# Optimization experiments

Measured on AMD Instinct MI355X. Metric: run time of the kernel, lower is better.

The kernel has to match this reference:

```python
import jax, jax.numpy as jnp
import numpy as np

N, L, I, H, D = 8192, 8, 256, 512, 8
PER = N // D  # nodes per depth level; level 0 nodes are tree roots


def setup_inputs() -> dict:
    key = jax.random.key(0)
    ks = jax.random.split(key, 9)
    s = 0.05
    x_seq = jax.random.normal(ks[0], (N, L, I), jnp.float32)
    # GRU params (torch nn.GRU layout, gate order r,z,n), stored transposed [in, 3H]
    W_ih = jax.random.normal(ks[1], (I, 3 * H), jnp.float32) * s
    W_hh = jax.random.normal(ks[2], (H, 3 * H), jnp.float32) * s
    b_ih = jax.random.normal(ks[3], (3 * H,), jnp.float32) * s
    b_hh = jax.random.normal(ks[4], (3 * H,), jnp.float32) * s
    # Child-sum TreeLSTM params: x-projections for i,o,u,f and recurrent U's
    Wx = jax.random.normal(ks[5], (H, 4 * H), jnp.float32) * s
    bx = jax.random.normal(ks[6], (4 * H,), jnp.float32) * s
    U_iou = jax.random.normal(ks[7], (H, 3 * H), jnp.float32) * s
    U_f = jax.random.normal(ks[8], (H, H), jnp.float32) * s
    # Forest structure: D levels of PER nodes; node at level d>0 has a random
    # parent at level d-1; roots (level 0) point at themselves (contribution is
    # zero because their own state is still zero when level 0 is processed).
    rng = np.random.default_rng(0)
    depth = np.repeat(np.arange(D), PER).astype(np.int32)
    parent = np.arange(N, dtype=np.int32)
    for d in range(1, D):
        parent[d * PER:(d + 1) * PER] = rng.integers((d - 1) * PER, d * PER, PER)
    root_ids = np.arange(PER, dtype=np.int32)
    return {
        "x_seq": x_seq, "W_ih": W_ih, "W_hh": W_hh, "b_ih": b_ih, "b_hh": b_hh,
        "Wx": Wx, "bx": bx, "U_iou": U_iou, "U_f": U_f,
        "parent": jnp.asarray(parent), "depth": jnp.asarray(depth),
        "root_ids": jnp.asarray(root_ids), "n_levels": D,
    }


def reference(x_seq, W_ih, W_hh, b_ih, b_hh, Wx, bx, U_iou, U_f,
              parent, depth, root_ids, n_levels):
    n = x_seq.shape[0]
    h_dim = W_hh.shape[0]

    # --- GRU over each node's encoding sequence (all nodes batched) ---
    def gru_step(h, x_t):  # h: [N,H], x_t: [N,I]
        gi = x_t @ W_ih + b_ih
        gh = h @ W_hh + b_hh
        ir, iz, inn = jnp.split(gi, 3, axis=-1)
        hr, hz, hn = jnp.split(gh, 3, axis=-1)
        r = jax.nn.sigmoid(ir + hr)
        z = jax.nn.sigmoid(iz + hz)
        ng = jnp.tanh(inn + r * hn)
        return (1.0 - z) * ng + z * h, None

    h0 = jnp.zeros((n, h_dim), x_seq.dtype)
    enc, _ = jax.lax.scan(gru_step, h0, jnp.swapaxes(x_seq, 0, 1))  # [N,H]

    # --- Child-sum TreeLSTM, processed leaves -> roots by depth level ---
    xg = enc @ Wx + bx  # [N,4H]
    xi, xo, xu, xf = jnp.split(xg, 4, axis=-1)
    c = jnp.zeros((n, h_dim), x_seq.dtype)
    h = jnp.zeros((n, h_dim), x_seq.dtype)
    for level in range(n_levels - 1, -1, -1):
        h_sum = jax.ops.segment_sum(h, parent, num_segments=n)  # sum over children
        giou = h_sum @ U_iou
        i = jax.nn.sigmoid(xi + giou[:, :h_dim])
        o = jax.nn.sigmoid(xo + giou[:, h_dim:2 * h_dim])
        u = jnp.tanh(xu + giou[:, 2 * h_dim:])
        # per-child forget gate uses parent's x projection and child's h
        f = jax.nn.sigmoid(xf[parent] + h @ U_f)
        fc = jax.ops.segment_sum(f * c, parent, num_segments=n)
        c_new = i * u + fc
        mask = (depth == level)[:, None]
        c = jnp.where(mask, c_new, c)
        h = jnp.where(mask, o * jnp.tanh(c_new), h)

    # root states per tree, stacked as [2, n_trees, H] -> (c_root, h_root)
    return jnp.stack([c[root_ids], h[root_ids]])
```

## Files before the change

### kernel.cpp

```cpp
#include <hip/hip_runtime.h>
#include <math.h>

typedef short bf16x8 __attribute__((ext_vector_type(8)));
typedef float f32x4 __attribute__((ext_vector_type(4)));

__device__ __forceinline__ float sigf(float x) {
    return __builtin_amdgcn_rcpf(1.f + __expf(-x));
}
__device__ __forceinline__ float tanhf_fast(float x) {
    const float e = __expf(2.f * x);
    return 1.f - 2.f * __builtin_amdgcn_rcpf(e + 1.f);
}

__device__ __forceinline__ unsigned short f2bf(float f) {
    union { float f; unsigned u; } v; v.f = f;
    unsigned r = (v.u + 0x7FFFu + ((v.u >> 16) & 1u)) >> 16;
    return (unsigned short)r;
}
__device__ __forceinline__ float bf2f(unsigned short u) {
    union { unsigned u; float f; } v; v.u = ((unsigned)u) << 16; return v.f;
}

__device__ __forceinline__ void gload16(const unsigned short* g, unsigned short* l) {
    __builtin_amdgcn_global_load_lds(
        (const __attribute__((address_space(1))) void*)g,
        (__attribute__((address_space(3))) void*)l, 16, 0, 0);
}

__device__ __forceinline__ int swz(int slot, int row) {
    return (slot ^ ((row >> 1) & 3)) * 8;
}

__global__ void cvt_f32_bf16(const float* __restrict__ src,
                             unsigned short* __restrict__ dst, int n)
{
    const int i = (blockIdx.x * blockDim.x + threadIdx.x) * 4;
    if (i >= n) return;
    const float4 v = *reinterpret_cast<const float4*>(src + i);
    ushort4 o;
    o.x = f2bf(v.x); o.y = f2bf(v.y); o.z = f2bf(v.z); o.w = f2bf(v.w);
    *reinterpret_cast<ushort4*>(dst + i) = o;
}

__global__ void transpose_cvt(const float* __restrict__ src,
                              unsigned short* __restrict__ dst,
                              int rows, int cols)
{
    __shared__ float tile[32][33];
    const int bc = blockIdx.x * 32, br = blockIdx.y * 32;
    const int tx = threadIdx.x, ty = threadIdx.y;
    #pragma unroll
    for (int i = 0; i < 32; i += 8)
        tile[ty + i][tx] = src[(size_t)(br + ty + i) * cols + bc + tx];
    __syncthreads();
    #pragma unroll
    for (int i = 0; i < 32; i += 8)
        dst[(size_t)(bc + ty + i) * rows + br + tx] = f2bf(tile[tx][ty + i]);
}

__global__ __launch_bounds__(256, 4)
void gru_mfma(const unsigned short* __restrict__ xb, int t,
              const unsigned short* __restrict__ hbi,
              unsigned short* __restrict__ hbo,
              const unsigned short* __restrict__ WihT,
              const unsigned short* __restrict__ WhhT,
              const float* __restrict__ b_ih, const float* __restrict__ b_hh)
{
    constexpr int I = 256, H = 512, LI = 2048;
    const int m0 = blockIdx.x * 64, j0 = blockIdx.y * 64;
    const int tid = (int)threadIdx.x, lane = tid & 63, wid = tid >> 6;
    const int wm = wid >> 1, wn = wid & 1;
    const int fr = lane & 15, kg = lane >> 4;
    const int lrow = lane >> 2;
    const int scol = swz(lane & 3, lrow);

    __shared__ unsigned short smem[2 * 8192];

    f32x4 ar[2][2], az[2][2], an[2][2], ah[2][2];
    #pragma unroll
    for (int i = 0; i < 2; ++i)
        #pragma unroll
        for (int j = 0; j < 2; ++j) {
            ar[i][j] = (f32x4){0.f, 0.f, 0.f, 0.f};
            az[i][j] = (f32x4){0.f, 0.f, 0.f, 0.f};
            an[i][j] = (f32x4){0.f, 0.f, 0.f, 0.f};
            ah[i][j] = (f32x4){0.f, 0.f, 0.f, 0.f};
        }

    constexpr int nkt1 = I / 32;
    constexpr int nkt = (I + H) / 32;

    auto stage = [&](int buf, int kt) {
        const bool s1 = (kt < nkt1);
        const int k0 = s1 ? kt * 32 : (kt - nkt1) * 32;
        unsigned short* base = &smem[buf * 8192];
        #pragma unroll
        for (int q = 0; q < 4; ++q) {
            const int c = wid * 4 + q;
            if (c < 4) {
                const int row = c * 16 + lrow;
                const unsigned short* g = s1
                    ? xb + (size_t)(m0 + row) * LI + t * I + k0 + scol
                    : hbi + (size_t)(m0 + row) * H + k0 + scol;
                gload16(g, base + c * 512);
            } else {
                const int bc = c - 4, gi = bc >> 2;
                const int row = (bc & 3) * 16 + lrow;
                const unsigned short* g = s1
                    ? WihT + (size_t)(gi * H + j0 + row) * I + k0 + scol
                    : WhhT + (size_t)(gi * H + j0 + row) * H + k0 + scol;
                gload16(g, base + c * 512);
            }
        }
    };

    stage(0, 0); stage(1, 1);

    for (int kt = 0; kt < nkt; ++kt) {
        if (kt + 1 < nkt) asm volatile("s_waitcnt vmcnt(4)" ::: "memory");
        else              asm volatile("s_waitcnt vmcnt(0)" ::: "memory");
        __builtin_amdgcn_s_barrier();

        const unsigned short* sb = &smem[(kt & 1) * 8192];
        bf16x8 af[2], bfr[2], bfz[2], bfn[2];
        #pragma unroll
        for (int mi = 0; mi < 2; ++mi) {
            const int row = wm * 32 + mi * 16 + fr;
            af[mi] = *reinterpret_cast<const bf16x8*>(&sb[row * 32 + swz(kg, row)]);
        }
        #pragma unroll
        for (int ni = 0; ni < 2; ++ni) {
            const int row = wn * 32 + ni * 16 + fr;
            const int sw = swz(kg, row);
            bfr[ni] = *reinterpret_cast<const bf16x8*>(&sb[2048 + (row) * 32 + sw]);
            bfz[ni] = *reinterpret_cast<const bf16x8*>(&sb[2048 + (64 + row) * 32 + sw]);
            bfn[ni] = *reinterpret_cast<const bf16x8*>(&sb[2048 + (128 + row) * 32 + sw]);
        }
        asm volatile("s_waitcnt lgkmcnt(0)" ::: "memory");
        __builtin_amdgcn_s_barrier();
        if (kt + 2 < nkt) stage(kt & 1, kt + 2);

        const bool p1 = (kt < nkt1);
        __builtin_amdgcn_s_setprio(1);
        #pragma unroll
        for (int mi = 0; mi < 2; ++mi)
            #pragma unroll
            for (int ni = 0; ni < 2; ++ni) {
                ar[mi][ni] = __builtin_amdgcn_mfma_f32_16x16x32_bf16(af[mi], bfr[ni], ar[mi][ni], 0, 0, 0);
                az[mi][ni] = __builtin_amdgcn_mfma_f32_16x16x32_bf16(af[mi], bfz[ni], az[mi][ni], 0, 0, 0);
                if (p1)
                    an[mi][ni] = __builtin_amdgcn_mfma_f32_16x16x32_bf16(af[mi], bfn[ni], an[mi][ni], 0, 0, 0);
                else
                    ah[mi][ni] = __builtin_amdgcn_mfma_f32_16x16x32_bf16(af[mi], bfn[ni], ah[mi][ni], 0, 0, 0);
            }
        __builtin_amdgcn_s_setprio(0);
    }

    #pragma unroll
    for (int ni = 0; ni < 2; ++ni) {
        const int j = j0 + wn * 32 + ni * 16 + fr;
        const float bir = b_ih[j],         bhr = b_hh[j];
        const float biz = b_ih[H + j],     bhz = b_hh[H + j];
        const float bin = b_ih[2 * H + j], bhn = b_hh[2 * H + j];
        #pragma unroll
        for (int mi = 0; mi < 2; ++mi) {
            #pragma unroll
            for (int r = 0; r < 4; ++r) {
                const int m = m0 + wm * 32 + mi * 16 + kg * 4 + r;
                const float rg = sigf(ar[mi][ni][r] + bir + bhr);
                const float zg = sigf(az[mi][ni][r] + biz + bhz);
                const float ng = tanhf_fast(an[mi][ni][r] + bin + rg * (ah[mi][ni][r] + bhn));
                const size_t off = (size_t)m * H + j;
                const float hv = bf2f(hbi[off]);
                hbo[off] = f2bf((1.f - zg) * ng + zg * hv);
            }
        }
    }
}

__global__ __launch_bounds__(256)
void mfma_gemm128(const unsigned short* __restrict__ A,
                  const unsigned short* __restrict__ BT,
                  const float* __restrict__ bias,
                  float* __restrict__ C, int M, int N, int K)
{
    const int m0 = blockIdx.x * 128, n0 = blockIdx.y * 128;
    const int tid = (int)threadIdx.x, lane = tid & 63, wid = tid >> 6;
    const int wm = wid >> 1, wn = wid & 1;
    const int fr = lane & 15, kg = lane >> 4;
    const int lrow = lane >> 2;
    const int scol = swz(lane & 3, lrow);

    __shared__ unsigned short smem[3 * 8192];

    f32x4 acc[4][4];
    #pragma unroll
    for (int i = 0; i < 4; ++i)
        #pragma unroll
        for (int j = 0; j < 4; ++j)
            acc[i][j] = (f32x4){0.f, 0.f, 0.f, 0.f};

    auto stage = [&](int buf, int kt) {
        const int k0 = kt * 32;
        unsigned short* base = &smem[buf * 8192];
        #pragma unroll
        for (int q = 0; q < 4; ++q) {
            const int c = wid * 4 + q;
            const unsigned short* g = (c < 8)
                ? A + (size_t)(m0 + c * 16 + lrow) * K + k0 + scol
                : BT + (size_t)(n0 + (c - 8) * 16 + lrow) * K + k0 + scol;
            gload16(g, base + c * 512);
        }
    };

    const int nkt = K >> 5;
    stage(0, 0); stage(1, 1); stage(2, 2);
    int cur = 0;

    for (int kt = 0; kt < nkt; ++kt) {
        if (kt + 2 < nkt)      asm volatile("s_waitcnt vmcnt(8)" ::: "memory");
        else if (kt + 1 < nkt) asm volatile("s_waitcnt vmcnt(4)" ::: "memory");
        else                   asm volatile("s_waitcnt vmcnt(0)" ::: "memory");
        __builtin_amdgcn_s_barrier();

        const unsigned short* sb = &smem[cur * 8192];
        bf16x8 af[4], bf[4];
        #pragma unroll
        for (int mi = 0; mi < 4; ++mi) {
            const int row = wm * 64 + mi * 16 + fr;
            af[mi] = *reinterpret_cast<const bf16x8*>(&sb[row * 32 + swz(kg, row)]);
        }
        #pragma unroll
        for (int ni = 0; ni < 4; ++ni) {
            const int row = wn * 64 + ni * 16 + fr;
            bf[ni] = *reinterpret_cast<const bf16x8*>(&sb[4096 + row * 32 + swz(kg, row)]);
        }
        asm volatile("s_waitcnt lgkmcnt(0)" ::: "memory");
        __builtin_amdgcn_s_barrier();
        if (kt + 3 < nkt) stage(cur, kt + 3);

        __builtin_amdgcn_s_setprio(1);
        #pragma unroll
        for (int mi = 0; mi < 4; ++mi)
            #pragma unroll
            for (int ni = 0; ni < 4; ++ni)
                acc[mi][ni] = __builtin_amdgcn_mfma_f32_16x16x32_bf16(
                    af[mi], bf[ni], acc[mi][ni], 0, 0, 0);
        __builtin_amdgcn_s_setprio(0);
        cur = (cur == 2) ? 0 : cur + 1;
    }

    #pragma unroll
    for (int ni = 0; ni < 4; ++ni) {
        const int n = n0 + wn * 64 + ni * 16 + fr;
        const float bv = bias ? bias[n] : 0.f;
        #pragma unroll
        for (int mi = 0; mi < 4; ++mi)
            #pragma unroll
            for (int r = 0; r < 4; ++r) {
                const int m = m0 + wm * 64 + mi * 16 + kg * 4 + r;
                C[(size_t)m * N + n] = acc[mi][ni][r] + bv;
            }
    }
}

__global__ __launch_bounds__(256, 4)
void tree_gemm(const unsigned short* __restrict__ hTb,
               const unsigned short* __restrict__ UcombT,
               const float* __restrict__ xg,
               const float* __restrict__ cT,
               const int* __restrict__ parent,
               int cstart, int pstart,
               float* __restrict__ giou,
               float* __restrict__ fcs)
{
    constexpr int H = 512, N4H = 2048, G3H = 1536;
    const int m0 = blockIdx.x * 64, n0 = blockIdx.y * 64;
    const int tid = (int)threadIdx.x, lane = tid & 63, wid = tid >> 6;
    const int wm = wid >> 1, wn = wid & 1;
    const int fr = lane & 15, kg = lane >> 4;
    const int lrow = lane >> 2;
    const int scol = swz(lane & 3, lrow);

    __shared__ unsigned short smem[3 * 4096];

    f32x4 acc[2][2];
    #pragma unroll
    for (int i = 0; i < 2; ++i)
        #pragma unroll
        for (int j = 0; j < 2; ++j)
            acc[i][j] = (f32x4){0.f, 0.f, 0.f, 0.f};

    auto stage = [&](int buf, int kt) {
        const int k0 = kt * 32;
        unsigned short* base = &smem[buf * 4096];
        #pragma unroll
        for (int q = 0; q < 2; ++q) {
            const int c = wid * 2 + q;
            const unsigned short* g = (c < 4)
                ? hTb + (size_t)(cstart + m0 + c * 16 + lrow) * H + k0 + scol
                : UcombT + (size_t)(n0 + (c - 4) * 16 + lrow) * H + k0 + scol;
            gload16(g, base + c * 512);
        }
    };

    constexpr int nkt = H / 32;
    stage(0, 0); stage(1, 1); stage(2, 2);
    int cur = 0;

    for (int kt = 0; kt < nkt; ++kt) {
        if (kt + 2 < nkt)      asm volatile("s_waitcnt vmcnt(4)" ::: "memory");
        else if (kt + 1 < nkt) asm volatile("s_waitcnt vmcnt(2)" ::: "memory");
        else                   asm volatile("s_waitcnt vmcnt(0)" ::: "memory");
        __builtin_amdgcn_s_barrier();

        const unsigned short* sb = &smem[cur * 4096];
        bf16x8 af[2], bf[2];
        #pragma unroll
        for (int mi = 0; mi < 2; ++mi) {
            const int row = wm * 32 + mi * 16 + fr;
            af[mi] = *reinterpret_cast<const bf16x8*>(&sb[row * 32 + swz(kg, row)]);
        }
        #pragma unroll
        for (int ni = 0; ni < 2; ++ni) {
            const int row = wn * 32 + ni * 16 + fr;
            bf[ni] = *reinterpret_cast<const bf16x8*>(&sb[2048 + row * 32 + swz(kg, row)]);
        }
        asm volatile("s_waitcnt lgkmcnt(0)" ::: "memory");
        __builtin_amdgcn_s_barrier();
        if (kt + 3 < nkt) stage(cur, kt + 3);

        __builtin_amdgcn_s_setprio(1);
        #pragma unroll
        for (int mi = 0; mi < 2; ++mi)
            #pragma unroll
            for (int ni = 0; ni < 2; ++ni)
                acc[mi][ni] = __builtin_amdgcn_mfma_f32_16x16x32_bf16(
                    af[mi], bf[ni], acc[mi][ni], 0, 0, 0);
        __builtin_amdgcn_s_setprio(0);
        cur = (cur == 2) ? 0 : cur + 1;
    }

    if (n0 < G3H) {
        #pragma unroll
        for (int mi = 0; mi < 2; ++mi)
            #pragma unroll
            for (int r = 0; r < 4; ++r) {
                const int m = m0 + wm * 32 + mi * 16 + kg * 4 + r;
                const int p = parent[cstart + m] - pstart;
                #pragma unroll
                for (int ni = 0; ni < 2; ++ni) {
                    const int n = n0 + wn * 32 + ni * 16 + fr;
                    atomicAdd(&giou[(size_t)p * G3H + n], acc[mi][ni][r]);
                }
            }
    } else {
        #pragma unroll
        for (int mi = 0; mi < 2; ++mi)
            #pragma unroll
            for (int r = 0; r < 4; ++r) {
                const int m = m0 + wm * 32 + mi * 16 + kg * 4 + r;
                const int child = cstart + m;
                const int p = parent[child];
                #pragma unroll
                for (int ni = 0; ni < 2; ++ni) {
                    const int jf = n0 + wn * 32 + ni * 16 + fr - G3H;
                    const float f = sigf(acc[mi][ni][r] + xg[(size_t)p * N4H + G3H + jf]);
                    atomicAdd(&fcs[(size_t)(p - pstart) * H + jf],
                              f * cT[(size_t)child * H + jf]);
                }
            }
    }
}

__global__ void level_update(const float* __restrict__ xg,
                             float* __restrict__ giou,
                             float* __restrict__ fcs,
                             float* __restrict__ cT, float* __restrict__ hT,
                             unsigned short* __restrict__ hb, int pstart)
{
    constexpr int H = 512, N4H = 2048, G3H = 1536;
    const int idx = blockIdx.x * blockDim.x + threadIdx.x;
    const int pi = idx >> 9, j = idx & (H - 1);
    const int p = pstart + pi;
    const size_t xb4 = (size_t)p * N4H;
    const size_t gb = (size_t)pi * G3H;
    const float ig = sigf(xg[xb4 + j] + giou[gb + j]);
    const float og = sigf(xg[xb4 + H + j] + giou[gb + H + j]);
    const float ug = tanhf_fast(xg[xb4 + 2 * H + j] + giou[gb + 2 * H + j]);
    const float cn = ig * ug + fcs[idx];
    const float hn = og * tanhf_fast(cn);
    const size_t off = (size_t)p * H + j;
    cT[off] = cn;
    hT[off] = hn;
    hb[off] = f2bf(hn);
    giou[gb + j] = 0.f;
    giou[gb + H + j] = 0.f;
    giou[gb + 2 * H + j] = 0.f;
    fcs[idx] = 0.f;
}

__global__ void gather_out_kernel(const float* __restrict__ c,
                                  const float* __restrict__ h,
                                  const int* __restrict__ root_ids,
                                  int nroot, float* __restrict__ out)
{
    constexpr int H = 512;
    const int idx = blockIdx.x * blockDim.x + threadIdx.x;
    const int t = idx >> 9, j = idx & (H - 1);
    const int rid = root_ids[t];
    out[idx] = c[(size_t)rid * H + j];
    out[(size_t)nroot * H + idx] = h[(size_t)rid * H + j];
}

extern "C" void kernel_launch(void* const* d_in, const int* in_sizes, int n_in,
                              void* d_out, int out_size, void* d_ws, size_t ws_size,
                              hipStream_t stream)
{
    const float* x_seq = (const float*)d_in[0];
    const float* W_ih  = (const float*)d_in[1];
    const float* W_hh  = (const float*)d_in[2];
    const float* b_ih  = (const float*)d_in[3];
    const float* b_hh  = (const float*)d_in[4];
    const float* Wx    = (const float*)d_in[5];
    const float* bx    = (const float*)d_in[6];
    const float* U_iou = (const float*)d_in[7];
    const float* U_f   = (const float*)d_in[8];
    const int* parent  = (const int*)d_in[9];
    const int* root_ids = (const int*)d_in[11];

    const int threeH = in_sizes[3];
    const int H   = threeH / 3;
    const int I   = in_sizes[1] / threeH;
    const int N   = in_sizes[9];
    const int L   = in_sizes[0] / (N * I);
    const int PER = in_sizes[11];
    const int D   = N / PER;

    const size_t NH = (size_t)N * H;
    const size_t PH = (size_t)PER * H;

    char* p = (char*)d_ws;
    const size_t zone_sz = ((size_t)N * 4 * H * 4 > (size_t)N * L * I * 2)
                         ? (size_t)N * 4 * H * 4 : (size_t)N * L * I * 2;
    unsigned short* xb = (unsigned short*)p;
    float* xg = (float*)p;                       p += zone_sz;
    unsigned short* hb0 = (unsigned short*)p;    p += NH * 2;
    unsigned short* hb1 = (unsigned short*)p;    p += NH * 2;
    float* cT = (float*)p;                       p += NH * 4;
    float* hT = (float*)p;                       p += NH * 4;
    unsigned short* WihT = (unsigned short*)p;   p += (size_t)threeH * I * 2;
    unsigned short* WhhT = (unsigned short*)p;   p += (size_t)threeH * H * 2;
    unsigned short* WxT  = (unsigned short*)p;   p += (size_t)4 * H * H * 2;
    unsigned short* UcombT = (unsigned short*)p; p += (size_t)4 * H * H * 2;
    float* giou = (float*)p;                     p += PH * 3 * 4;
    float* fcs  = (float*)p;                     p += PH * 4;
    if ((size_t)(p - (char*)d_ws) > ws_size) return;

    {
        const int n = N * L * I;
        cvt_f32_bf16<<<(n / 4 + 255) / 256, 256, 0, stream>>>(x_seq, xb, n);
        dim3 blk(32, 8);
        transpose_cvt<<<dim3(threeH / 32, I / 32), blk, 0, stream>>>(W_ih, WihT, I, threeH);
        transpose_cvt<<<dim3(threeH / 32, H / 32), blk, 0, stream>>>(W_hh, WhhT, H, threeH);
        transpose_cvt<<<dim3(4 * H / 32, H / 32), blk, 0, stream>>>(Wx, WxT, H, 4 * H);
        transpose_cvt<<<dim3(threeH / 32, H / 32), blk, 0, stream>>>(U_iou, UcombT, H, threeH);
        transpose_cvt<<<dim3(H / 32, H / 32), blk, 0, stream>>>(
            U_f, UcombT + (size_t)threeH * H, H, H);
    }
    hipMemsetAsync(hb0, 0, NH * 2, stream);
    hipMemsetAsync(giou, 0, PH * 4 * 4, stream);

    {
        dim3 grid(N / 64, H / 64);
        for (int t = 0; t < L; ++t) {
            const unsigned short* hin = (t & 1) ? hb1 : hb0;
            unsigned short* hout = (t & 1) ? hb0 : hb1;
            gru_mfma<<<grid, 256, 0, stream>>>(xb, t, hin, hout,
                                               WihT, WhhT, b_ih, b_hh);
        }
    }

    mfma_gemm128<<<dim3(N / 128, 4 * H / 128), 256, 0, stream>>>(
        hb0, WxT, bx, xg, N, 4 * H, H);

    unsigned short* hTb = hb1;
    const int pw_blocks = (int)(PH / 256);

    for (int lvl = D - 1; lvl >= 0; --lvl) {
        const int pstart = lvl * PER;
        const int cstart = (lvl + 1) * PER;

        if (lvl < D - 1)
            tree_gemm<<<dim3(PER / 64, (4 * H) / 64), 256, 0, stream>>>(
                hTb, UcombT, xg, cT, parent, cstart, pstart, giou, fcs);

        level_update<<<pw_blocks, 256, 0, stream>>>(xg, giou, fcs, cT, hT,
                                                    hTb, pstart);
    }

    gather_out_kernel<<<pw_blocks, 256, 0, stream>>>(cT, hT, root_ids, PER,
                                                     (float*)d_out);
}
```

Before: 504.0 us.

## Hoist GRU input projection into one batched GEMM and store projections in bf16

```diff
diff --git a/kernel.cpp b/kernel.cpp
--- a/kernel.cpp
+++ b/kernel.cpp
@@ -29,6 +29,9 @@
 
 __device__ __forceinline__ int swz(int slot, int row) {
     return (slot ^ ((row >> 1) & 3)) * 8;
+}
+__device__ __forceinline__ int tix(int ml, int jl) {
+    return ((ml >> 4) * 2 + (jl >> 5)) * 512 + (ml & 15) * 32 + (jl & 31);
 }
 
 __global__ void cvt_f32_bf16(const float* __restrict__ src,
@@ -58,57 +61,145 @@
         dst[(size_t)(bc + ty + i) * rows + br + tx] = f2bf(tile[tx][ty + i]);
 }
 
+__global__ __launch_bounds__(256)
+void gemm_bf16out(const unsigned short* __restrict__ A,
+                  const unsigned short* __restrict__ BT,
+                  const float* __restrict__ bias,
+                  unsigned short* __restrict__ Cb, int M, int N, int K)
+{
+    const int m0 = blockIdx.x * 128, n0 = blockIdx.y * 128;
+    const int tid = (int)threadIdx.x, lane = tid & 63, wid = tid >> 6;
+    const int wm = wid >> 1, wn = wid & 1;
+    const int fr = lane & 15, kg = lane >> 4;
+    const int lrow = lane >> 2;
+    const int scol = swz(lane & 3, lrow);
+
+    __shared__ unsigned short smem[3 * 8192];
+
+    f32x4 acc[4][4];
+    #pragma unroll
+    for (int i = 0; i < 4; ++i)
+        #pragma unroll
+        for (int j = 0; j < 4; ++j)
+            acc[i][j] = (f32x4){0.f, 0.f, 0.f, 0.f};
+
+    auto stage = [&](int buf, int kt) {
+        const int k0 = kt * 32;
+        unsigned short* base = &smem[buf * 8192];
+        #pragma unroll
+        for (int q = 0; q < 4; ++q) {
+            const int c = wid * 4 + q;
+            const unsigned short* g = (c < 8)
+                ? A + (size_t)(m0 + c * 16 + lrow) * K + k0 + scol
+                : BT + (size_t)(n0 + (c - 8) * 16 + lrow) * K + k0 + scol;
+            gload16(g, base + c * 512);
+        }
+    };
+
+    const int nkt = K >> 5;
+    stage(0, 0); stage(1, 1); stage(2, 2);
+    int cur = 0;
+
+    for (int kt = 0; kt < nkt; ++kt) {
+        if (kt + 2 < nkt)      asm volatile("s_waitcnt vmcnt(8)" ::: "memory");
+        else if (kt + 1 < nkt) asm volatile("s_waitcnt vmcnt(4)" ::: "memory");
+        else                   asm volatile("s_waitcnt vmcnt(0)" ::: "memory");
+        __builtin_amdgcn_s_barrier();
+
+        const unsigned short* sb = &smem[cur * 8192];
+        bf16x8 af[4], bf[4];
+        #pragma unroll
+        for (int mi = 0; mi < 4; ++mi) {
+            const int row = wm * 64 + mi * 16 + fr;
+            af[mi] = *reinterpret_cast<const bf16x8*>(&sb[row * 32 + swz(kg, row)]);
+        }
+        #pragma unroll
+        for (int ni = 0; ni < 4; ++ni) {
+            const int row = wn * 64 + ni * 16 + fr;
+            bf[ni] = *reinterpret_cast<const bf16x8*>(&sb[4096 + row * 32 + swz(kg, row)]);
+        }
+        asm volatile("s_waitcnt lgkmcnt(0)" ::: "memory");
+        __builtin_amdgcn_s_barrier();
+        if (kt + 3 < nkt) stage(cur, kt + 3);
+
+        __builtin_amdgcn_s_setprio(1);
+        #pragma unroll
+        for (int mi = 0; mi < 4; ++mi)
+            #pragma unroll
+            for (int ni = 0; ni < 4; ++ni)
+                acc[mi][ni] = __builtin_amdgcn_mfma_f32_16x16x32_bf16(
+                    af[mi], bf[ni], acc[mi][ni], 0, 0, 0);
+        __builtin_amdgcn_s_setprio(0);
+        cur = (cur == 2) ? 0 : cur + 1;
+    }
+
+    #pragma unroll
+    for (int ni = 0; ni < 4; ++ni) {
+        const int nl = wn * 64 + ni * 16 + fr;
+        const float bv = bias[n0 + nl];
+        #pragma unroll
+        for (int mi = 0; mi < 4; ++mi)
+            #pragma unroll
+            for (int r = 0; r < 4; ++r) {
+                const int ml = wm * 64 + mi * 16 + kg * 4 + r;
+                smem[ml * 128 + nl] = f2bf(acc[mi][ni][r] + bv);
+            }
+    }
+    __syncthreads();
+    #pragma unroll
+    for (int e = 0; e < 8; ++e) {
+        const int id = tid + e * 256;
+        const int row = id >> 4, cw = id & 15;
+        const int4 v = *reinterpret_cast<const int4*>(&smem[row * 128 + cw * 8]);
+        *reinterpret_cast<int4*>(&Cb[(size_t)(m0 + row) * N + n0 + cw * 8]) = v;
+    }
+}
+
 __global__ __launch_bounds__(256, 4)
-void gru_mfma(const unsigned short* __restrict__ xb, int t,
+void gru_step(const unsigned short* __restrict__ gi,
+              int t,
               const unsigned short* __restrict__ hbi,
               unsigned short* __restrict__ hbo,
-              const unsigned short* __restrict__ WihT,
               const unsigned short* __restrict__ WhhT,
-              const float* __restrict__ b_ih, const float* __restrict__ b_hh)
-{
-    constexpr int I = 256, H = 512, LI = 2048;
+              const float* __restrict__ b_hh)
+{
+    constexpr int H = 512, G3H = 1536, L = 8;
     const int m0 = blockIdx.x * 64, j0 = blockIdx.y * 64;
     const int tid = (int)threadIdx.x, lane = tid & 63, wid = tid >> 6;
     const int wm = wid >> 1, wn = wid & 1;
     const int fr = lane & 15, kg = lane >> 4;
     const int lrow = lane >> 2;
     const int scol = swz(lane & 3, lrow);
+    const int ucol = (lane & 3) * 8;
 
     __shared__ unsigned short smem[2 * 8192];
 
-    f32x4 ar[2][2], az[2][2], an[2][2], ah[2][2];
+    f32x4 ar[2][2], az[2][2], ah[2][2];
     #pragma unroll
     for (int i = 0; i < 2; ++i)
         #pragma unroll
         for (int j = 0; j < 2; ++j) {
             ar[i][j] = (f32x4){0.f, 0.f, 0.f, 0.f};
             az[i][j] = (f32x4){0.f, 0.f, 0.f, 0.f};
-            an[i][j] = (f32x4){0.f, 0.f, 0.f, 0.f};
             ah[i][j] = (f32x4){0.f, 0.f, 0.f, 0.f};
         }
 
-    constexpr int nkt1 = I / 32;
-    constexpr int nkt = (I + H) / 32;
+    constexpr int nkt = H / 32;
 
     auto stage = [&](int buf, int kt) {
-        const bool s1 = (kt < nkt1);
-        const int k0 = s1 ? kt * 32 : (kt - nkt1) * 32;
+        const int k0 = kt * 32;
         unsigned short* base = &smem[buf * 8192];
         #pragma unroll
         for (int q = 0; q < 4; ++q) {
             const int c = wid * 4 + q;
             if (c < 4) {
-                const int row = c * 16 + lrow;
-                const unsigned short* g = s1
-                    ? xb + (size_t)(m0 + row) * LI + t * I + k0 + scol
-                    : hbi + (size_t)(m0 + row) * H + k0 + scol;
+                const unsigned short* g =
+                    hbi + (size_t)(m0 + c * 16 + lrow) * H + k0 + scol;
                 gload16(g, base + c * 512);
             } else {
-                const int bc = c - 4, gi = bc >> 2;
-                const int row = (bc & 3) * 16 + lrow;
-                const unsigned short* g = s1
-                    ? WihT + (size_t)(gi * H + j0 + row) * I + k0 + scol
-                    : WhhT + (size_t)(gi * H + j0 + row) * H + k0 + scol;
+                const int gate = (c - 4) >> 2, rowg = (c - 4) & 3;
+                const unsigned short* g =
+                    WhhT + (size_t)(gate * H + j0 + rowg * 16 + lrow) * H + k0 + scol;
                 gload16(g, base + c * 512);
             }
         }
@@ -140,7 +231,6 @@
         __builtin_amdgcn_s_barrier();
         if (kt + 2 < nkt) stage(kt & 1, kt + 2);
 
-        const bool p1 = (kt < nkt1);
         __builtin_amdgcn_s_setprio(1);
         #pragma unroll
         for (int mi = 0; mi < 2; ++mi)
@@ -148,126 +238,83 @@
             for (int ni = 0; ni < 2; ++ni) {
                 ar[mi][ni] = __builtin_amdgcn_mfma_f32_16x16x32_bf16(af[mi], bfr[ni], ar[mi][ni], 0, 0, 0);
                 az[mi][ni] = __builtin_amdgcn_mfma_f32_16x16x32_bf16(af[mi], bfz[ni], az[mi][ni], 0, 0, 0);
-                if (p1)
-                    an[mi][ni] = __builtin_amdgcn_mfma_f32_16x16x32_bf16(af[mi], bfn[ni], an[mi][ni], 0, 0, 0);
-                else
-                    ah[mi][ni] = __builtin_amdgcn_mfma_f32_16x16x32_bf16(af[mi], bfn[ni], ah[mi][ni], 0, 0, 0);
+                ah[mi][ni] = __builtin_amdgcn_mfma_f32_16x16x32_bf16(af[mi], bfn[ni], ah[mi][ni], 0, 0, 0);
             }
         __builtin_amdgcn_s_setprio(0);
     }
 
     #pragma unroll
+    for (int q = 0; q < 8; ++q) {
+        const int c = wid * 8 + q;
+        if (c < 24) {
+            const int g = c >> 3, cc = c & 7;
+            const int rowg = cc >> 1, colg = cc & 1;
+            const unsigned short* src = gi
+                + ((size_t)(m0 + rowg * 16 + lrow) * L + t) * G3H
+                + g * H + j0 + colg * 32 + ucol;
+            gload16(src, &smem[g * 4096 + cc * 512]);
+        } else {
+            const int cc = c - 24;
+            const int rowg = cc >> 1, colg = cc & 1;
+            const unsigned short* src = hbi
+                + (size_t)(m0 + rowg * 16 + lrow) * H + j0 + colg * 32 + ucol;
+            gload16(src, &smem[12288 + cc * 512]);
+        }
+    }
+    __syncthreads();
+
+    unsigned short res[2][2][4];
+    #pragma unroll
     for (int ni = 0; ni < 2; ++ni) {
-        const int j = j0 + wn * 32 + ni * 16 + fr;
-        const float bir = b_ih[j],         bhr = b_hh[j];
-        const float biz = b_ih[H + j],     bhz = b_hh[H + j];
-        const float bin = b_ih[2 * H + j], bhn = b_hh[2 * H + j];
+        const int jl = wn * 32 + ni * 16 + fr;
+        const int j = j0 + jl;
+        const float bhr = b_hh[j], bhz = b_hh[H + j], bhn = b_hh[2 * H + j];
         #pragma unroll
         for (int mi = 0; mi < 2; ++mi) {
             #pragma unroll
             for (int r = 0; r < 4; ++r) {
-                const int m = m0 + wm * 32 + mi * 16 + kg * 4 + r;
-                const float rg = sigf(ar[mi][ni][r] + bir + bhr);
-                const float zg = sigf(az[mi][ni][r] + biz + bhz);
-                const float ng = tanhf_fast(an[mi][ni][r] + bin + rg * (ah[mi][ni][r] + bhn));
-                const size_t off = (size_t)m * H + j;
-                const float hv = bf2f(hbi[off]);
-                hbo[off] = f2bf((1.f - zg) * ng + zg * hv);
-            }
-        }
-    }
-}
-
-__global__ __launch_bounds__(256)
-void mfma_gemm128(const unsigned short* __restrict__ A,
-                  const unsigned short* __restrict__ BT,
-                  const float* __restrict__ bias,
-                  float* __restrict__ C, int M, int N, int K)
-{
-    const int m0 = blockIdx.x * 128, n0 = blockIdx.y * 128;
-    const int tid = (int)threadIdx.x, lane = tid & 63, wid = tid >> 6;
-    const int wm = wid >> 1, wn = wid & 1;
-    const int fr = lane & 15, kg = lane >> 4;
-    const int lrow = lane >> 2;
-    const int scol = swz(lane & 3, lrow);
-
-    __shared__ unsigned short smem[3 * 8192];
-
-    f32x4 acc[4][4];
-    #pragma unroll
-    for (int i = 0; i < 4; ++i)
-        #pragma unroll
-        for (int j = 0; j < 4; ++j)
-            acc[i][j] = (f32x4){0.f, 0.f, 0.f, 0.f};
-
-    auto stage = [&](int buf, int kt) {
-        const int k0 = kt * 32;
-        unsigned short* base = &smem[buf * 8192];
-        #pragma unroll
-        for (int q = 0; q < 4; ++q) {
-            const int c = wid * 4 + q;
-            const unsigned short* g = (c < 8)
-                ? A + (size_t)(m0 + c * 16 + lrow) * K + k0 + scol
-                : BT + (size_t)(n0 + (c - 8) * 16 + lrow) * K + k0 + scol;
-            gload16(g, base + c * 512);
-        }
-    };
-
-    const int nkt = K >> 5;
-    stage(0, 0); stage(1, 1); stage(2, 2);
-    int cur = 0;
-
-    for (int kt = 0; kt < nkt; ++kt) {
-        if (kt + 2 < nkt)      asm volatile("s_waitcnt vmcnt(8)" ::: "memory");
-        else if (kt + 1 < nkt) asm volatile("s_waitcnt vmcnt(4)" ::: "memory");
-        else                   asm volatile("s_waitcnt vmcnt(0)" ::: "memory");
-        __builtin_amdgcn_s_barrier();
-
-        const unsigned short* sb = &smem[cur * 8192];
-        bf16x8 af[4], bf[4];
-        #pragma unroll
-        for (int mi = 0; mi < 4; ++mi) {
-            const int row = wm * 64 + mi * 16 + fr;
-            af[mi] = *reinterpret_cast<const bf16x8*>(&sb[row * 32 + swz(kg, row)]);
-        }
-        #pragma unroll
-        for (int ni = 0; ni < 4; ++ni) {
-            const int row = wn * 64 + ni * 16 + fr;
-            bf[ni] = *reinterpret_cast<const bf16x8*>(&sb[4096 + row * 32 + swz(kg, row)]);
-        }
-        asm volatile("s_waitcnt lgkmcnt(0)" ::: "memory");
-        __builtin_amdgcn_s_barrier();
-        if (kt + 3 < nkt) stage(cur, kt + 3);
-
-        __builtin_amdgcn_s_setprio(1);
-        #pragma unroll
-        for (int mi = 0; mi < 4; ++mi)
-            #pragma unroll
-            for (int ni = 0; ni < 4; ++ni)
-                acc[mi][ni] = __builtin_amdgcn_mfma_f32_16x16x32_bf16(
-                    af[mi], bf[ni], acc[mi][ni], 0, 0, 0);
-        __builtin_amdgcn_s_setprio(0);
-        cur = (cur == 2) ? 0 : cur + 1;
-    }
-
-    #pragma unroll
-    for (int ni = 0; ni < 4; ++ni) {
-        const int n = n0 + wn * 64 + ni * 16 + fr;
-        const float bv = bias ? bias[n] : 0.f;
-        #pragma unroll
-        for (int mi = 0; mi < 4; ++mi)
+                const int ml = wm * 32 + mi * 16 + kg * 4 + r;
+                const int ix = tix(ml, jl);
+                const float gr = bf2f(smem[ix]);
+                const float gz = bf2f(smem[4096 + ix]);
+                const float gn = bf2f(smem[8192 + ix]);
+                const float hv = bf2f(smem[12288 + ix]);
+                const float rg = sigf(ar[mi][ni][r] + gr + bhr);
+                const float zg = sigf(az[mi][ni][r] + gz + bhz);
+                const float ng = tanhf_fast(gn + rg * (ah[mi][ni][r] + bhn));
+                res[ni][mi][r] = f2bf((1.f - zg) * ng + zg * hv);
+            }
+        }
+    }
+    __syncthreads();
+
+    #pragma unroll
+    for (int ni = 0; ni < 2; ++ni) {
+        const int jl = wn * 32 + ni * 16 + fr;
+        #pragma unroll
+        for (int mi = 0; mi < 2; ++mi)
             #pragma unroll
             for (int r = 0; r < 4; ++r) {
-                const int m = m0 + wm * 64 + mi * 16 + kg * 4 + r;
-                C[(size_t)m * N + n] = acc[mi][ni][r] + bv;
-            }
+                const int ml = wm * 32 + mi * 16 + kg * 4 + r;
+                smem[tix(ml, jl)] = res[ni][mi][r];
+            }
+    }
+    __syncthreads();
+
+    #pragma unroll
+    for (int e = 0; e < 2; ++e) {
+        const int id = tid + e * 256;
+        const int ml = id >> 3, jw = id & 7;
+        const int4 v = *reinterpret_cast<const int4*>(
+            &smem[((ml >> 4) * 2 + (jw >> 2)) * 512 + (ml & 15) * 32 + (jw & 3) * 8]);
+        *reinterpret_cast<int4*>(&hbo[(size_t)(m0 + ml) * H + j0 + jw * 8]) = v;
     }
 }
 
 __global__ __launch_bounds__(256, 4)
 void tree_gemm(const unsigned short* __restrict__ hTb,
                const unsigned short* __restrict__ UcombT,
-               const float* __restrict__ xg,
+               const unsigned short* __restrict__ xgb,
                const float* __restrict__ cT,
                const int* __restrict__ parent,
                int cstart, int pstart,
@@ -365,7 +412,8 @@
                 #pragma unroll
                 for (int ni = 0; ni < 2; ++ni) {
                     const int jf = n0 + wn * 32 + ni * 16 + fr - G3H;
-                    const float f = sigf(acc[mi][ni][r] + xg[(size_t)p * N4H + G3H + jf]);
+                    const float f = sigf(acc[mi][ni][r] +
+                                         bf2f(xgb[(size_t)p * N4H + G3H + jf]));
                     atomicAdd(&fcs[(size_t)(p - pstart) * H + jf],
                               f * cT[(size_t)child * H + jf]);
                 }
@@ -373,7 +421,7 @@
     }
 }
 
-__global__ void level_update(const float* __restrict__ xg,
+__global__ void level_update(const unsigned short* __restrict__ xgb,
                              float* __restrict__ giou,
                              float* __restrict__ fcs,
                              float* __restrict__ cT, float* __restrict__ hT,
@@ -385,9 +433,9 @@
     const int p = pstart + pi;
     const size_t xb4 = (size_t)p * N4H;
     const size_t gb = (size_t)pi * G3H;
-    const float ig = sigf(xg[xb4 + j] + giou[gb + j]);
-    const float og = sigf(xg[xb4 + H + j] + giou[gb + H + j]);
-    const float ug = tanhf_fast(xg[xb4 + 2 * H + j] + giou[gb + 2 * H + j]);
+    const float ig = sigf(bf2f(xgb[xb4 + j]) + giou[gb + j]);
+    const float og = sigf(bf2f(xgb[xb4 + H + j]) + giou[gb + H + j]);
+    const float ug = tanhf_fast(bf2f(xgb[xb4 + 2 * H + j]) + giou[gb + 2 * H + j]);
     const float cn = ig * ug + fcs[idx];
     const float hn = og * tanhf_fast(cn);
     const size_t off = (size_t)p * H + j;
@@ -441,21 +489,23 @@
     const size_t PH = (size_t)PER * H;
 
     char* p = (char*)d_ws;
-    const size_t zone_sz = ((size_t)N * 4 * H * 4 > (size_t)N * L * I * 2)
-                         ? (size_t)N * 4 * H * 4 : (size_t)N * L * I * 2;
-    unsigned short* xb = (unsigned short*)p;
-    float* xg = (float*)p;                       p += zone_sz;
+    const size_t xb_sz  = (size_t)N * L * I * 2;
+    const size_t xgb_sz = (size_t)N * 4 * H * 2;
+    const size_t zone_sz = xb_sz > xgb_sz ? xb_sz : xgb_sz;
+    unsigned short* xb  = (unsigned short*)p;
+    unsigned short* xgb = (unsigned short*)p;    p += zone_sz;
+    unsigned short* gi  = (unsigned short*)p;    p += (size_t)N * L * threeH * 2;
     unsigned short* hb0 = (unsigned short*)p;    p += NH * 2;
     unsigned short* hb1 = (unsigned short*)p;    p += NH * 2;
-    float* cT = (float*)p;                       p += NH * 4;
-    float* hT = (float*)p;                       p += NH * 4;
     unsigned short* WihT = (unsigned short*)p;   p += (size_t)threeH * I * 2;
     unsigned short* WhhT = (unsigned short*)p;   p += (size_t)threeH * H * 2;
     unsigned short* WxT  = (unsigned short*)p;   p += (size_t)4 * H * H * 2;
     unsigned short* UcombT = (unsigned short*)p; p += (size_t)4 * H * H * 2;
-    float* giou = (float*)p;                     p += PH * 3 * 4;
-    float* fcs  = (float*)p;                     p += PH * 4;
     if ((size_t)(p - (char*)d_ws) > ws_size) return;
+    float* cT   = (float*)gi;
+    float* hT   = cT + NH;
+    float* giou = hT + NH;
+    float* fcs  = giou + PH * 3;
 
     {
         const int n = N * L * I;
@@ -468,22 +518,25 @@
         transpose_cvt<<<dim3(H / 32, H / 32), blk, 0, stream>>>(
             U_f, UcombT + (size_t)threeH * H, H, H);
     }
+
+    gemm_bf16out<<<dim3(N * L / 128, threeH / 128), 256, 0, stream>>>(
+        xb, WihT, b_ih, gi, N * L, threeH, I);
+
     hipMemsetAsync(hb0, 0, NH * 2, stream);
-    hipMemsetAsync(giou, 0, PH * 4 * 4, stream);
 
     {
         dim3 grid(N / 64, H / 64);
         for (int t = 0; t < L; ++t) {
             const unsigned short* hin = (t & 1) ? hb1 : hb0;
             unsigned short* hout = (t & 1) ? hb0 : hb1;
-            gru_mfma<<<grid, 256, 0, stream>>>(xb, t, hin, hout,
-                                               WihT, WhhT, b_ih, b_hh);
-        }
-    }
-
-    mfma_gemm128<<<dim3(N / 128, 4 * H / 128), 256, 0, stream>>>(
-        hb0, WxT, bx, xg, N, 4 * H, H);
-
+            gru_step<<<grid, 256, 0, stream>>>(gi, t, hin, hout, WhhT, b_hh);
+        }
+    }
+
+    gemm_bf16out<<<dim3(N / 128, 4 * H / 128), 256, 0, stream>>>(
+        hb0, WxT, bx, xgb, N, 4 * H, H);
+
+    hipMemsetAsync(giou, 0, PH * 4 * 4, stream);
     unsigned short* hTb = hb1;
     const int pw_blocks = (int)(PH / 256);
 
@@ -493,9 +546,9 @@
 
         if (lvl < D - 1)
             tree_gemm<<<dim3(PER / 64, (4 * H) / 64), 256, 0, stream>>>(
-                hTb, UcombT, xg, cT, parent, cstart, pstart, giou, fcs);
-
-        level_update<<<pw_blocks, 256, 0, stream>>>(xg, giou, fcs, cT, hT,
+                hTb, UcombT, xgb, cT, parent, cstart, pstart, giou, fcs);
+
+        level_update<<<pw_blocks, 256, 0, stream>>>(xgb, giou, fcs, cT, hT,
                                                     hTb, pstart);
     }
 
```

Result: slower. 514.2 us (+2.0%).
